# Kernel tuning notes

Hardware: AMD Instinct MI355X
Metric: run time of the kernel (lower is better)

The kernel has to match this reference:

```python
import jax, jax.numpy as jnp
import numpy as np


def setup_inputs() -> dict:
    key = jax.random.key(0)
    k1, k2, k3 = jax.random.split(key, 3)
    B, S, D, O, C = 4, 1024, 1024, 1024, 8
    x = jax.random.normal(k1, (B, S, D), dtype=jnp.float32)
    category_id = jax.random.randint(k2, (B, S), 0, C, dtype=jnp.int64)
    weight = jax.random.normal(k3, (C, D, O), dtype=jnp.float32)
    bias = jnp.zeros((C, O), dtype=jnp.float32)
    return {"x": x, "category_id": category_id, "weight": weight, "bias": bias}


def reference(x, category_id, weight, bias):
    # Faithful to: out[t] = x[t] @ weight[cid[t]] + bias[cid[t]]
    # Instead of gathering a full [T, D, O] per-token weight tensor (the torch
    # original's bmm formulation), compute x against every category's matrix and
    # select the row for each token's category -- same math, far less memory.
    orig_shape = x.shape
    T = np.prod(orig_shape[:-1])
    x_flat = x.reshape(T, orig_shape[-1])            # [T, D]
    cid = category_id.reshape(T)                      # [T]
    y_all = jnp.einsum('td,cdo->tco', x_flat, weight)  # [T, C, O]
    y = jnp.take_along_axis(y_all, cid[:, None, None], axis=1)[:, 0, :]  # [T, O]
    out = y + bias[cid]                               # [T, O]
    return out.reshape(*orig_shape[:-1], out.shape[-1])
```

## Files before the change

### kernel.cpp

```cpp
#include <hip/hip_runtime.h>


typedef __attribute__((ext_vector_type(8))) short bf16x8;
typedef __attribute__((ext_vector_type(4))) float f32x4;
typedef __attribute__((ext_vector_type(8))) unsigned short ushort8_t;

__device__ __forceinline__ unsigned short f2bf(float f) {
  unsigned u = __float_as_uint(f);
  u += 0x7FFFu + ((u >> 16) & 1u);
  return (unsigned short)(u >> 16);
}

__device__ __forceinline__ void gload_lds16(const unsigned short* g, unsigned short* l) {
  __builtin_amdgcn_global_load_lds(
      (const __attribute__((address_space(1))) unsigned int*)g,
      (__attribute__((address_space(3))) unsigned int*)l, 16, 0, 0);
}

#define MAXC 8

__global__ void k_prep(const float* __restrict__ W, unsigned short* __restrict__ Wt,
                       int Dd, int Oo,
                       const float* __restrict__ x, unsigned short* __restrict__ xb, int nX,
                       const int* __restrict__ cid, int* __restrict__ counts,
                       int* __restrict__ bucket, int T, int C, int tpw) {
  int b   = blockIdx.x;
  int tid = threadIdx.x;

  if (b == 0) {
    __shared__ int cnt[256][MAXC];
    int tpt = (T + 255) / 256;
    int t0  = tid * tpt;
    int t1  = min(t0 + tpt, T);
    for (int c = 0; c < C; ++c) cnt[tid][c] = 0;
    for (int t = t0; t < t1; ++t) cnt[tid][cid[t]]++;
    __syncthreads();
    if (tid < C) {
      int run = 0;
      for (int t = 0; t < 256; ++t) { int v = cnt[t][tid]; cnt[t][tid] = run; run += v; }
      counts[tid] = run;
    }
    __syncthreads();
    for (int t = t0; t < t1; ++t) {
      int c = cid[t];
      int p = cnt[tid][c]++;
      bucket[c * T + p] = t;
    }
    return;
  }

  if (b > tpw) {
    int i = ((b - tpw - 1) * 256 + tid) * 8;
    if (i >= nX) return;
    float4 a0 = *reinterpret_cast<const float4*>(x + i);
    float4 a1 = *reinterpret_cast<const float4*>(x + i + 4);
    ushort8_t o;
    o[0] = f2bf(a0.x); o[1] = f2bf(a0.y); o[2] = f2bf(a0.z); o[3] = f2bf(a0.w);
    o[4] = f2bf(a1.x); o[5] = f2bf(a1.y); o[6] = f2bf(a1.z); o[7] = f2bf(a1.w);
    *reinterpret_cast<ushort8_t*>(xb + i) = o;
    return;
  }

  int bb  = b - 1;
  int tpc = (Dd / 64) * (Oo / 64);
  int c   = bb / tpc;
  int rem = bb % tpc;
  int d0  = (rem / (Oo / 64)) * 64;
  int o0  = (rem % (Oo / 64)) * 64;

  __shared__ float t[64][65];
  const float* Wc = W + (size_t)c * Dd * Oo;
#pragma unroll
  for (int p = 0; p < 4; ++p) {
    int chunk = p * 256 + tid;
    int r  = chunk >> 4;
    int cb = chunk & 15;
    float4 v = *reinterpret_cast<const float4*>(Wc + (size_t)(d0 + r) * Oo + o0 + cb * 4);
    t[r][cb * 4 + 0] = v.x; t[r][cb * 4 + 1] = v.y;
    t[r][cb * 4 + 2] = v.z; t[r][cb * 4 + 3] = v.w;
  }
  __syncthreads();
  unsigned short* Wtc = Wt + (size_t)c * Oo * Dd;
#pragma unroll
  for (int p = 0; p < 2; ++p) {
    int chunk = p * 256 + tid;
    int orow = chunk >> 3;
    int dseg = chunk & 7;
    ushort8_t w;
#pragma unroll
    for (int j = 0; j < 8; ++j) w[j] = f2bf(t[dseg * 8 + j][orow]);
    *reinterpret_cast<ushort8_t*>(Wtc + (size_t)(o0 + orow) * Dd + d0 + dseg * 8) = w;
  }
}

#define BM 128
#define BN 128
#define BK 64
#define TILE_A (BM * BK)
#define TILE_B (BN * BK)

__global__ __launch_bounds__(1024) void k_ggemm(
    const unsigned short* __restrict__ xb, const unsigned short* __restrict__ Wt,
    const float* __restrict__ bias, const int* __restrict__ counts,
    const int* __restrict__ bucket, float* __restrict__ out,
    int T, int Dd, int Oo) {
  int c  = blockIdx.x;
  int Mc = counts[c];
  int m0 = blockIdx.z * BM;
  if (m0 >= Mc) return;
  int n0 = blockIdx.y * BN;

  extern __shared__ __align__(16) unsigned short smem[];
  unsigned short* Al = smem;
  unsigned short* Bl = smem + 3 * TILE_A;

  const int tid  = threadIdx.x;
  const int lane = tid & 63;
  const int wid  = tid >> 6;
  const int wm   = wid >> 2, wn = wid & 3;

  const int* buck = bucket + c * T;
  const unsigned short* Wc = Wt + (size_t)c * Oo * Dd;

  const unsigned short* aSrc;
  const unsigned short* bSrc;
  int sOff;
  {
    int row = wid * 8 + (lane >> 3);
    int seg = (lane & 7) ^ (row & 7);
    int mr  = m0 + row;
    int tok = buck[mr < Mc ? mr : Mc - 1];
    aSrc = xb + (size_t)tok * Dd + seg * 8;
    bSrc = Wc + (size_t)(n0 + row) * Dd + seg * 8;
    sOff = (wid * 8) * BK;
  }

  const f32x4 fzero = {0.f, 0.f, 0.f, 0.f};
  f32x4 acc[2][2];
#pragma unroll
  for (int i = 0; i < 2; ++i)
#pragma unroll
    for (int j = 0; j < 2; ++j) acc[i][j] = fzero;

  const int KT = Dd / BK;

#pragma unroll
  for (int t8 = 0; t8 < 2; ++t8) {
    int ko = t8 * BK;
    gload_lds16(aSrc + ko, Al + t8 * TILE_A + sOff);
    gload_lds16(bSrc + ko, Bl + t8 * TILE_B + sOff);
  }

  int cur = 0;
  for (int kt = 0; kt < KT; ++kt) {
    asm volatile("s_waitcnt lgkmcnt(0)" ::: "memory");
    if (kt < KT - 1) {
      asm volatile("s_waitcnt vmcnt(2)" ::: "memory");
    } else {
      asm volatile("s_waitcnt vmcnt(0)" ::: "memory");
    }
    __builtin_amdgcn_sched_barrier(0);
    __builtin_amdgcn_s_barrier();
    __builtin_amdgcn_sched_barrier(0);

    if (kt + 2 < KT) {
      int nb = cur + 2; if (nb >= 3) nb -= 3;
      int ko = (kt + 2) * BK;
      gload_lds16(aSrc + ko, Al + nb * TILE_A + sOff);
      gload_lds16(bSrc + ko, Bl + nb * TILE_B + sOff);
    }

    const unsigned short* Ac = Al + cur * TILE_A;
    const unsigned short* Bc = Bl + cur * TILE_B;
#pragma unroll
    for (int kk = 0; kk < 2; ++kk) {
      bf16x8 af[2], bf[2];
#pragma unroll
      for (int mi = 0; mi < 2; ++mi) {
        int row  = wm * 32 + mi * 16 + (lane & 15);
        int slot = (kk * 4 + (lane >> 4)) ^ (row & 7);
        af[mi] = *reinterpret_cast<const bf16x8*>(&Ac[row * BK + slot * 8]);
      }
#pragma unroll
      for (int ni = 0; ni < 2; ++ni) {
        int row  = wn * 32 + ni * 16 + (lane & 15);
        int slot = (kk * 4 + (lane >> 4)) ^ (row & 7);
        bf[ni] = *reinterpret_cast<const bf16x8*>(&Bc[row * BK + slot * 8]);
      }
#pragma unroll
      for (int mi = 0; mi < 2; ++mi)
#pragma unroll
        for (int ni = 0; ni < 2; ++ni)
          acc[mi][ni] = __builtin_amdgcn_mfma_f32_16x16x32_bf16(af[mi], bf[ni], acc[mi][ni], 0, 0, 0);
    }
    cur = (cur + 1 == 3) ? 0 : cur + 1;
  }

#pragma unroll
  for (int mi = 0; mi < 2; ++mi) {
    int rb = m0 + wm * 32 + mi * 16 + (lane >> 4) * 4;
#pragma unroll
    for (int r = 0; r < 4; ++r) {
      int mrow = rb + r;
      if (mrow < Mc) {
        int tok = buck[mrow];
        float* orow = out + (size_t)tok * Oo;
#pragma unroll
        for (int ni = 0; ni < 2; ++ni) {
          int col = n0 + wn * 32 + ni * 16 + (lane & 15);
          orow[col] = acc[mi][ni][r] + bias[c * Oo + col];
        }
      }
    }
  }
}

extern "C" void kernel_launch(void* const* d_in, const int* in_sizes, int n_in,
                              void* d_out, int out_size, void* d_ws, size_t ws_size,
                              hipStream_t stream) {
  const float* x    = (const float*)d_in[0];
  const int*   cid  = (const int*)d_in[1];
  const float* W    = (const float*)d_in[2];
  const float* bias = (const float*)d_in[3];
  float* out = (float*)d_out;

  int T = in_sizes[1];
  int D = in_sizes[0] / T;
  int O = out_size / T;
  int C = in_sizes[3] / O;

  char* ws = (char*)d_ws;
  int* counts = (int*)ws;
  int* bucket = (int*)(ws + 64);
  unsigned short* xb = (unsigned short*)(ws + 64 + (size_t)C * T * 4);
  unsigned short* Wt = xb + (size_t)T * D;

  int tpw  = C * (D / 64) * (O / 64);
  int cvtb = (T * D / 8 + 255) / 256;
  k_prep<<<1 + tpw + cvtb, 256, 0, stream>>>(W, Wt, D, O, x, xb, T * D,
                                             cid, counts, bucket, T, C, tpw);
  size_t ldsBytes = (size_t)3 * (TILE_A + TILE_B) * sizeof(unsigned short);
  k_ggemm<<<dim3(C, O / BN, (T + BM - 1) / BM), 1024, ldsBytes, stream>>>(
      xb, Wt, bias, counts, bucket, out, T, D, O);
}
```

Before: 46.74 us.

## Split-K grouped GEMM with atomic accumulation and double-buffered LDS

Splits the K dimension of the per-category GEMM in two, doubling the grid. Partial results are accumulated into the output with float atomicAdd, and bias is added only by the first split. The output is zeroed inside the prep kernel, and the LDS pipeline drops from triple to double buffering with static shared memory. This targets low occupancy and wave quantization from the many nearly empty per-category tiles, at the cost of atomic traffic, an extra output zeroing pass, and less load/compute overlap.

```diff
diff --git a/kernel.cpp b/kernel.cpp
--- a/kernel.cpp
+++ b/kernel.cpp
@@ -23,7 +23,8 @@
                        int Dd, int Oo,
                        const float* __restrict__ x, unsigned short* __restrict__ xb, int nX,
                        const int* __restrict__ cid, int* __restrict__ counts,
-                       int* __restrict__ bucket, int T, int C, int tpw) {
+                       int* __restrict__ bucket, int T, int C, int tpw, int cvtb,
+                       float* __restrict__ outZ, int nOut) {
   int b   = blockIdx.x;
   int tid = threadIdx.x;
 
@@ -49,6 +50,15 @@
     return;
   }
 
+  if (b > tpw + cvtb) {
+    int i = ((b - tpw - cvtb - 1) * 256 + tid) * 8;
+    if (i >= nOut) return;
+    float4 z = {0.f, 0.f, 0.f, 0.f};
+    *reinterpret_cast<float4*>(outZ + i)     = z;
+    *reinterpret_cast<float4*>(outZ + i + 4) = z;
+    return;
+  }
+
   if (b > tpw) {
     int i = ((b - tpw - 1) * 256 + tid) * 8;
     if (i >= nX) return;
@@ -96,23 +106,24 @@
 #define BM 128
 #define BN 128
 #define BK 64
+#define KSPLIT 2
 #define TILE_A (BM * BK)
 #define TILE_B (BN * BK)
 
-__global__ __launch_bounds__(1024) void k_ggemm(
+__global__ __launch_bounds__(1024, 8) void k_ggemm(
     const unsigned short* __restrict__ xb, const unsigned short* __restrict__ Wt,
     const float* __restrict__ bias, const int* __restrict__ counts,
     const int* __restrict__ bucket, float* __restrict__ out,
     int T, int Dd, int Oo) {
   int c  = blockIdx.x;
   int Mc = counts[c];
-  int m0 = blockIdx.z * BM;
+  int kz = blockIdx.z & (KSPLIT - 1);
+  int m0 = (blockIdx.z >> 1) * BM;
   if (m0 >= Mc) return;
   int n0 = blockIdx.y * BN;
 
-  extern __shared__ __align__(16) unsigned short smem[];
-  unsigned short* Al = smem;
-  unsigned short* Bl = smem + 3 * TILE_A;
+  __shared__ __align__(16) unsigned short Al[2][TILE_A];
+  __shared__ __align__(16) unsigned short Bl[2][TILE_B];
 
   const int tid  = threadIdx.x;
   const int lane = tid & 63;
@@ -121,6 +132,7 @@
 
   const int* buck = bucket + c * T;
   const unsigned short* Wc = Wt + (size_t)c * Oo * Dd;
+  const int kbase = kz * (Dd / KSPLIT);
 
   const unsigned short* aSrc;
   const unsigned short* bSrc;
@@ -130,8 +142,8 @@
     int seg = (lane & 7) ^ (row & 7);
     int mr  = m0 + row;
     int tok = buck[mr < Mc ? mr : Mc - 1];
-    aSrc = xb + (size_t)tok * Dd + seg * 8;
-    bSrc = Wc + (size_t)(n0 + row) * Dd + seg * 8;
+    aSrc = xb + (size_t)tok * Dd + kbase + seg * 8;
+    bSrc = Wc + (size_t)(n0 + row) * Dd + kbase + seg * 8;
     sOff = (wid * 8) * BK;
   }
 
@@ -142,36 +154,21 @@
 #pragma unroll
     for (int j = 0; j < 2; ++j) acc[i][j] = fzero;
 
-  const int KT = Dd / BK;
-
-#pragma unroll
-  for (int t8 = 0; t8 < 2; ++t8) {
-    int ko = t8 * BK;
-    gload_lds16(aSrc + ko, Al + t8 * TILE_A + sOff);
-    gload_lds16(bSrc + ko, Bl + t8 * TILE_B + sOff);
-  }
-
-  int cur = 0;
+  const int KT = Dd / BK / KSPLIT;
+
+  gload_lds16(aSrc, Al[0] + sOff);
+  gload_lds16(bSrc, Bl[0] + sOff);
+  asm volatile("s_waitcnt vmcnt(0)" ::: "memory");
+  __builtin_amdgcn_sched_barrier(0);
+  __builtin_amdgcn_s_barrier();
+
   for (int kt = 0; kt < KT; ++kt) {
-    asm volatile("s_waitcnt lgkmcnt(0)" ::: "memory");
-    if (kt < KT - 1) {
-      asm volatile("s_waitcnt vmcnt(2)" ::: "memory");
-    } else {
-      asm volatile("s_waitcnt vmcnt(0)" ::: "memory");
-    }
-    __builtin_amdgcn_sched_barrier(0);
-    __builtin_amdgcn_s_barrier();
-    __builtin_amdgcn_sched_barrier(0);
-
-    if (kt + 2 < KT) {
-      int nb = cur + 2; if (nb >= 3) nb -= 3;
-      int ko = (kt + 2) * BK;
-      gload_lds16(aSrc + ko, Al + nb * TILE_A + sOff);
-      gload_lds16(bSrc + ko, Bl + nb * TILE_B + sOff);
-    }
-
-    const unsigned short* Ac = Al + cur * TILE_A;
-    const unsigned short* Bc = Bl + cur * TILE_B;
+    int cur = kt & 1;
+    if (kt + 1 < KT) {
+      int ko = (kt + 1) * BK;
+      gload_lds16(aSrc + ko, Al[cur ^ 1] + sOff);
+      gload_lds16(bSrc + ko, Bl[cur ^ 1] + sOff);
+    }
 #pragma unroll
     for (int kk = 0; kk < 2; ++kk) {
       bf16x8 af[2], bf[2];
@@ -179,13 +176,13 @@
       for (int mi = 0; mi < 2; ++mi) {
         int row  = wm * 32 + mi * 16 + (lane & 15);
         int slot = (kk * 4 + (lane >> 4)) ^ (row & 7);
-        af[mi] = *reinterpret_cast<const bf16x8*>(&Ac[row * BK + slot * 8]);
+        af[mi] = *reinterpret_cast<const bf16x8*>(&Al[cur][row * BK + slot * 8]);
       }
 #pragma unroll
       for (int ni = 0; ni < 2; ++ni) {
         int row  = wn * 32 + ni * 16 + (lane & 15);
         int slot = (kk * 4 + (lane >> 4)) ^ (row & 7);
-        bf[ni] = *reinterpret_cast<const bf16x8*>(&Bc[row * BK + slot * 8]);
+        bf[ni] = *reinterpret_cast<const bf16x8*>(&Bl[cur][row * BK + slot * 8]);
       }
 #pragma unroll
       for (int mi = 0; mi < 2; ++mi)
@@ -193,7 +190,11 @@
         for (int ni = 0; ni < 2; ++ni)
           acc[mi][ni] = __builtin_amdgcn_mfma_f32_16x16x32_bf16(af[mi], bf[ni], acc[mi][ni], 0, 0, 0);
     }
-    cur = (cur + 1 == 3) ? 0 : cur + 1;
+    if (kt + 1 < KT) {
+      asm volatile("s_waitcnt vmcnt(0)" ::: "memory");
+      __builtin_amdgcn_sched_barrier(0);
+      __builtin_amdgcn_s_barrier();
+    }
   }
 
 #pragma unroll
@@ -208,7 +209,8 @@
 #pragma unroll
         for (int ni = 0; ni < 2; ++ni) {
           int col = n0 + wn * 32 + ni * 16 + (lane & 15);
-          orow[col] = acc[mi][ni][r] + bias[c * Oo + col];
+          float v = acc[mi][ni][r] + (kz == 0 ? bias[c * Oo + col] : 0.f);
+          atomicAdd(&orow[col], v);
         }
       }
     }
@@ -237,9 +239,10 @@
 
   int tpw  = C * (D / 64) * (O / 64);
   int cvtb = (T * D / 8 + 255) / 256;
-  k_prep<<<1 + tpw + cvtb, 256, 0, stream>>>(W, Wt, D, O, x, xb, T * D,
-                                             cid, counts, bucket, T, C, tpw);
-  size_t ldsBytes = (size_t)3 * (TILE_A + TILE_B) * sizeof(unsigned short);
-  k_ggemm<<<dim3(C, O / BN, (T + BM - 1) / BM), 1024, ldsBytes, stream>>>(
+  int zb   = (out_size / 8 + 255) / 256;
+  k_prep<<<1 + tpw + cvtb + zb, 256, 0, stream>>>(W, Wt, D, O, x, xb, T * D,
+                                                  cid, counts, bucket, T, C, tpw, cvtb,
+                                                  out, out_size);
+  k_ggemm<<<dim3(C, O / BN, KSPLIT * ((T + BM - 1) / BM)), 1024, 0, stream>>>(
       xb, Wt, bias, counts, bucket, out, T, D, O);
 }
```

Measured after the change: 70.77 us. +51.4%, slower.

## Load gathered A fragments directly from global into registers, bypassing LDS

Applied to the files above, without the earlier changes.

The A operand (gathered token rows of bf16 x) is no longer staged through LDS. Each lane instead loads its MFMA fragment straight from global memory into registers, prefetching one half-tile ahead, while only the weight tile B keeps the triple-buffered LDS pipeline. This halves LDS footprint and removes the A-side LDS writes and reads. In exchange, A loads are 16-byte per-lane global reads with less coalescing, are duplicated across the 4 wn waves, and their latency is exposed with only a short prefetch distance. The existing vmcnt waits also now count these extra loads.

```diff
diff --git a/kernel.cpp b/kernel.cpp
--- a/kernel.cpp
+++ b/kernel.cpp
@@ -96,7 +96,6 @@
 #define BM 128
 #define BN 128
 #define BK 64
-#define TILE_A (BM * BK)
 #define TILE_B (BN * BK)
 
 __global__ __launch_bounds__(1024) void k_ggemm(
@@ -110,9 +109,7 @@
   if (m0 >= Mc) return;
   int n0 = blockIdx.y * BN;
 
-  extern __shared__ __align__(16) unsigned short smem[];
-  unsigned short* Al = smem;
-  unsigned short* Bl = smem + 3 * TILE_A;
+  __shared__ __align__(16) unsigned short Bl[3][TILE_B];
 
   const int tid  = threadIdx.x;
   const int lane = tid & 63;
@@ -122,17 +119,21 @@
   const int* buck = bucket + c * T;
   const unsigned short* Wc = Wt + (size_t)c * Oo * Dd;
 
-  const unsigned short* aSrc;
   const unsigned short* bSrc;
-  int sOff;
+  int bOff;
   {
     int row = wid * 8 + (lane >> 3);
     int seg = (lane & 7) ^ (row & 7);
-    int mr  = m0 + row;
-    int tok = buck[mr < Mc ? mr : Mc - 1];
-    aSrc = xb + (size_t)tok * Dd + seg * 8;
     bSrc = Wc + (size_t)(n0 + row) * Dd + seg * 8;
-    sOff = (wid * 8) * BK;
+    bOff = (wid * 8) * BK;
+  }
+
+  const unsigned short* aB[2];
+#pragma unroll
+  for (int mi = 0; mi < 2; ++mi) {
+    int mrow = m0 + wm * 32 + mi * 16 + (lane & 15);
+    int tok  = buck[mrow < Mc ? mrow : Mc - 1];
+    aB[mi] = xb + (size_t)tok * Dd + (lane >> 4) * 8;
   }
 
   const f32x4 fzero = {0.f, 0.f, 0.f, 0.f};
@@ -144,15 +145,15 @@
 
   const int KT = Dd / BK;
 
-#pragma unroll
-  for (int t8 = 0; t8 < 2; ++t8) {
-    int ko = t8 * BK;
-    gload_lds16(aSrc + ko, Al + t8 * TILE_A + sOff);
-    gload_lds16(bSrc + ko, Bl + t8 * TILE_B + sOff);
-  }
-
-  int cur = 0;
+  gload_lds16(bSrc,      Bl[0] + bOff);
+  gload_lds16(bSrc + BK, Bl[1] + bOff);
+  bf16x8 a0[2], a1[2];
+  a0[0] = *reinterpret_cast<const bf16x8*>(aB[0]);
+  a0[1] = *reinterpret_cast<const bf16x8*>(aB[1]);
+
   for (int kt = 0; kt < KT; ++kt) {
+    int cur = kt % 3;
+    int ko  = kt * BK;
     asm volatile("s_waitcnt lgkmcnt(0)" ::: "memory");
     if (kt < KT - 1) {
       asm volatile("s_waitcnt vmcnt(2)" ::: "memory");
@@ -163,37 +164,45 @@
     __builtin_amdgcn_s_barrier();
     __builtin_amdgcn_sched_barrier(0);
 
+    a1[0] = *reinterpret_cast<const bf16x8*>(aB[0] + ko + 32);
+    a1[1] = *reinterpret_cast<const bf16x8*>(aB[1] + ko + 32);
     if (kt + 2 < KT) {
-      int nb = cur + 2; if (nb >= 3) nb -= 3;
-      int ko = (kt + 2) * BK;
-      gload_lds16(aSrc + ko, Al + nb * TILE_A + sOff);
-      gload_lds16(bSrc + ko, Bl + nb * TILE_B + sOff);
-    }
-
-    const unsigned short* Ac = Al + cur * TILE_A;
-    const unsigned short* Bc = Bl + cur * TILE_B;
-#pragma unroll
-    for (int kk = 0; kk < 2; ++kk) {
-      bf16x8 af[2], bf[2];
-#pragma unroll
-      for (int mi = 0; mi < 2; ++mi) {
-        int row  = wm * 32 + mi * 16 + (lane & 15);
-        int slot = (kk * 4 + (lane >> 4)) ^ (row & 7);
-        af[mi] = *reinterpret_cast<const bf16x8*>(&Ac[row * BK + slot * 8]);
-      }
+      int nb = (kt + 2) % 3;
+      gload_lds16(bSrc + (kt + 2) * BK, Bl[nb] + bOff);
+    }
+
+    {
+      bf16x8 bf[2];
 #pragma unroll
       for (int ni = 0; ni < 2; ++ni) {
         int row  = wn * 32 + ni * 16 + (lane & 15);
-        int slot = (kk * 4 + (lane >> 4)) ^ (row & 7);
-        bf[ni] = *reinterpret_cast<const bf16x8*>(&Bc[row * BK + slot * 8]);
+        int slot = (lane >> 4) ^ (row & 7);
+        bf[ni] = *reinterpret_cast<const bf16x8*>(&Bl[cur][row * BK + slot * 8]);
       }
 #pragma unroll
       for (int mi = 0; mi < 2; ++mi)
 #pragma unroll
         for (int ni = 0; ni < 2; ++ni)
-          acc[mi][ni] = __builtin_amdgcn_mfma_f32_16x16x32_bf16(af[mi], bf[ni], acc[mi][ni], 0, 0, 0);
-    }
-    cur = (cur + 1 == 3) ? 0 : cur + 1;
+          acc[mi][ni] = __builtin_amdgcn_mfma_f32_16x16x32_bf16(a0[mi], bf[ni], acc[mi][ni], 0, 0, 0);
+    }
+    if (kt + 1 < KT) {
+      a0[0] = *reinterpret_cast<const bf16x8*>(aB[0] + ko + BK);
+      a0[1] = *reinterpret_cast<const bf16x8*>(aB[1] + ko + BK);
+    }
+    {
+      bf16x8 bf[2];
+#pragma unroll
+      for (int ni = 0; ni < 2; ++ni) {
+        int row  = wn * 32 + ni * 16 + (lane & 15);
+        int slot = (4 + (lane >> 4)) ^ (row & 7);
+        bf[ni] = *reinterpret_cast<const bf16x8*>(&Bl[cur][row * BK + slot * 8]);
+      }
+#pragma unroll
+      for (int mi = 0; mi < 2; ++mi)
+#pragma unroll
+        for (int ni = 0; ni < 2; ++ni)
+          acc[mi][ni] = __builtin_amdgcn_mfma_f32_16x16x32_bf16(a1[mi], bf[ni], acc[mi][ni], 0, 0, 0);
+    }
   }
 
 #pragma unroll
@@ -239,7 +248,6 @@
   int cvtb = (T * D / 8 + 255) / 256;
   k_prep<<<1 + tpw + cvtb, 256, 0, stream>>>(W, Wt, D, O, x, xb, T * D,
                                              cid, counts, bucket, T, C, tpw);
-  size_t ldsBytes = (size_t)3 * (TILE_A + TILE_B) * sizeof(unsigned short);
-  k_ggemm<<<dim3(C, O / BN, (T + BM - 1) / BM), 1024, ldsBytes, stream>>>(
+  k_ggemm<<<dim3(C, O / BN, (T + BM - 1) / BM), 1024, 0, stream>>>(
       xb, Wt, bias, counts, bucket, out, T, D, O);
 }
```

Result: slower. 70.48 us (+50.8%).

## Split GEMM k-step into two barrier-separated halves with staggered loads and setprio

Applied to the files above, without the earlier changes.

Each K-tile iteration of the grouped GEMM now runs as two half-steps separated by an extra workgroup barrier. The A-tile prefetch is issued before the first half and the B-tile prefetch before the second, and the MFMA blocks are wrapped in s_setprio to raise wave priority during matrix math. The bias values are also loaded into registers once before the main loop instead of being read per output element. The aim is to interleave global-to-LDS traffic with MFMA work and cut epilogue loads, at the cost of one more barrier per iteration across the 16 waves of each block.

```diff
diff --git a/kernel.cpp b/kernel.cpp
--- a/kernel.cpp
+++ b/kernel.cpp
@@ -135,6 +135,11 @@
     sOff = (wid * 8) * BK;
   }
 
+  float bias_r[2];
+#pragma unroll
+  for (int ni = 0; ni < 2; ++ni)
+    bias_r[ni] = bias[c * Oo + n0 + wn * 32 + ni * 16 + (lane & 15)];
+
   const f32x4 fzero = {0.f, 0.f, 0.f, 0.f};
   f32x4 acc[2][2];
 #pragma unroll
@@ -151,8 +156,8 @@
     gload_lds16(bSrc + ko, Bl + t8 * TILE_B + sOff);
   }
 
-  int cur = 0;
   for (int kt = 0; kt < KT; ++kt) {
+    int cur = kt % 3;
     asm volatile("s_waitcnt lgkmcnt(0)" ::: "memory");
     if (kt < KT - 1) {
       asm volatile("s_waitcnt vmcnt(2)" ::: "memory");
@@ -163,37 +168,56 @@
     __builtin_amdgcn_s_barrier();
     __builtin_amdgcn_sched_barrier(0);
 
-    if (kt + 2 < KT) {
-      int nb = cur + 2; if (nb >= 3) nb -= 3;
-      int ko = (kt + 2) * BK;
-      gload_lds16(aSrc + ko, Al + nb * TILE_A + sOff);
-      gload_lds16(bSrc + ko, Bl + nb * TILE_B + sOff);
-    }
-
-    const unsigned short* Ac = Al + cur * TILE_A;
-    const unsigned short* Bc = Bl + cur * TILE_B;
-#pragma unroll
-    for (int kk = 0; kk < 2; ++kk) {
+    int nb = (cur + 2 >= 3) ? cur - 1 : cur + 2;
+    if (kt + 2 < KT) gload_lds16(aSrc + (kt + 2) * BK, Al + nb * TILE_A + sOff);
+    {
       bf16x8 af[2], bf[2];
 #pragma unroll
       for (int mi = 0; mi < 2; ++mi) {
         int row  = wm * 32 + mi * 16 + (lane & 15);
-        int slot = (kk * 4 + (lane >> 4)) ^ (row & 7);
-        af[mi] = *reinterpret_cast<const bf16x8*>(&Ac[row * BK + slot * 8]);
+        int slot = (lane >> 4) ^ (row & 7);
+        af[mi] = *reinterpret_cast<const bf16x8*>(&Al[cur * TILE_A + row * BK + slot * 8]);
       }
 #pragma unroll
       for (int ni = 0; ni < 2; ++ni) {
         int row  = wn * 32 + ni * 16 + (lane & 15);
-        int slot = (kk * 4 + (lane >> 4)) ^ (row & 7);
-        bf[ni] = *reinterpret_cast<const bf16x8*>(&Bc[row * BK + slot * 8]);
-      }
+        int slot = (lane >> 4) ^ (row & 7);
+        bf[ni] = *reinterpret_cast<const bf16x8*>(&Bl[cur * TILE_B + row * BK + slot * 8]);
+      }
+      __builtin_amdgcn_s_setprio(1);
 #pragma unroll
       for (int mi = 0; mi < 2; ++mi)
 #pragma unroll
         for (int ni = 0; ni < 2; ++ni)
           acc[mi][ni] = __builtin_amdgcn_mfma_f32_16x16x32_bf16(af[mi], bf[ni], acc[mi][ni], 0, 0, 0);
-    }
-    cur = (cur + 1 == 3) ? 0 : cur + 1;
+      __builtin_amdgcn_s_setprio(0);
+    }
+    __builtin_amdgcn_sched_barrier(0);
+    __builtin_amdgcn_s_barrier();
+    __builtin_amdgcn_sched_barrier(0);
+    if (kt + 2 < KT) gload_lds16(bSrc + (kt + 2) * BK, Bl + nb * TILE_B + sOff);
+    {
+      bf16x8 af[2], bf[2];
+#pragma unroll
+      for (int mi = 0; mi < 2; ++mi) {
+        int row  = wm * 32 + mi * 16 + (lane & 15);
+        int slot = (4 + (lane >> 4)) ^ (row & 7);
+        af[mi] = *reinterpret_cast<const bf16x8*>(&Al[cur * TILE_A + row * BK + slot * 8]);
+      }
+#pragma unroll
+      for (int ni = 0; ni < 2; ++ni) {
+        int row  = wn * 32 + ni * 16 + (lane & 15);
+        int slot = (4 + (lane >> 4)) ^ (row & 7);
+        bf[ni] = *reinterpret_cast<const bf16x8*>(&Bl[cur * TILE_B + row * BK + slot * 8]);
+      }
+      __builtin_amdgcn_s_setprio(1);
+#pragma unroll
+      for (int mi = 0; mi < 2; ++mi)
+#pragma unroll
+        for (int ni = 0; ni < 2; ++ni)
+          acc[mi][ni] = __builtin_amdgcn_mfma_f32_16x16x32_bf16(af[mi], bf[ni], acc[mi][ni], 0, 0, 0);
+      __builtin_amdgcn_s_setprio(0);
+    }
   }
 
 #pragma unroll
@@ -208,7 +232,7 @@
 #pragma unroll
         for (int ni = 0; ni < 2; ++ni) {
           int col = n0 + wn * 32 + ni * 16 + (lane & 15);
-          orow[col] = acc[mi][ni][r] + bias[c * Oo + col];
+          orow[col] = acc[mi][ni][r] + bias_r[ni];
         }
       }
     }
```

Result: slower. 48.47 us (+3.7%).
